# Kernel optimization log

Hardware: AMD Instinct MI355X
Metric: run time of the kernel (lower is better)

The kernel has to match this reference:

```python
import jax, jax.numpy as jnp
import numpy as np
import math

DIM = 512
HEADS = 8
HEAD_DIM = DIM // HEADS
WINDOW = 16
HIDDEN = 4 * DIM
SCALE = HEAD_DIM ** (-0.5)


def _best_hw(n):
    r = int(math.sqrt(n))
    best = (1, n)
    min_gap = n - 1
    for h in range(1, r + 1):
        if n % h == 0:
            w = n // h
            if abs(w - h) < min_gap:
                min_gap = abs(w - h)
                best = (h, w)
    return best


def _pad_to_window(x, w):
    # x: [B,C,H,W]
    B, C, H, W = x.shape
    ph = (-H) % w
    pw = (-W) % w
    if ph or pw:
        x = jnp.pad(x, ((0, 0), (0, 0), (0, ph), (0, pw)))
    return x, (ph, pw)


def _window_partition(x, w):
    # [B,C,Hp,Wp] -> [B*nW, w*w, C]
    B, C, Hp, Wp = x.shape
    x = x.reshape(B, C, Hp // w, w, Wp // w, w)
    x = jnp.transpose(x, (0, 2, 4, 3, 5, 1))  # [B,nWh,nWw,w,w,C]
    return x.reshape(-1, w * w, C), (Hp, Wp, Hp // w, Wp // w)


def _window_reverse(windows, w, meta):
    Hp, Wp, nWh, nWw = meta
    B = windows.shape[0] // (nWh * nWw)
    C = windows.shape[-1]
    x = windows.reshape(B, nWh, nWw, w, w, C)
    x = jnp.transpose(x, (0, 5, 1, 3, 2, 4))
    return x.reshape(B, C, Hp, Wp)


def _branch(src, oth, Wq, bq, Wk, bk, Wv, bv, Wo, bo, W1, b1, W2, b2):
    # src acts as query grid; oth is resized onto src's grid (cross attention)
    B, N, C = src.shape
    Hs, Ws = _best_hw(N)
    src_map = jnp.transpose(src, (0, 2, 1)).reshape(B, C, Hs, Ws)
    M = oth.shape[1]
    Ho, Wo_sp = _best_hw(M)
    oth_map = jnp.transpose(oth, (0, 2, 1)).reshape(B, C, Ho, Wo_sp)
    # bilinear resize, half-pixel centers (== torch align_corners=False, no antialias)
    oth_rs = jax.image.resize(oth_map, (B, C, Hs, Ws), method='bilinear', antialias=False)

    src_pad, (ph, pw) = _pad_to_window(src_map, WINDOW)
    oth_pad, _ = _pad_to_window(oth_rs, WINDOW)
    src_win, meta = _window_partition(src_pad, WINDOW)   # [Bn,T,C]
    oth_win, _ = _window_partition(oth_pad, WINDOW)

    q = src_win @ Wq + bq
    k = oth_win @ Wk + bk
    v = src_win @ Wv + bv
    Bn, T, _ = q.shape
    q = q.reshape(Bn, T, HEADS, HEAD_DIM)
    k = k.reshape(Bn, T, HEADS, HEAD_DIM)
    v = v.reshape(Bn, T, HEADS, HEAD_DIM)
    attn = jnp.einsum('bthd,bshd->bhts', q, k) * SCALE
    attn = jax.nn.softmax(attn, axis=-1)  # dropout is identity in eval
    out = jnp.einsum('bhts,bshd->bthd', attn, v).reshape(Bn, T, C)
    out = out @ Wo + bo

    out_map = _window_reverse(out, WINDOW, meta)
    Hp, Wp = out_map.shape[-2:]
    if ph or pw:
        out_map = out_map[:, :, :Hp - ph, :Wp - pw]
    tokens = jnp.transpose(out_map.reshape(B, C, -1), (0, 2, 1)) + src
    # MLP (GELU exact, dropout identity)
    h = jax.nn.gelu(tokens @ W1 + b1, approximate=False)
    tokens = (h @ W2 + b2) + tokens
    return tokens


def setup_inputs() -> dict:
    key = jax.random.key(0)
    ks = jax.random.split(key, 16)
    s = 0.02
    return {
        'x': jax.random.normal(ks[0], (8, 4096, DIM), jnp.float32),
        'y': jax.random.normal(ks[1], (8, 1024, DIM), jnp.float32),
        'Wq': jax.random.normal(ks[2], (DIM, DIM), jnp.float32) * s,
        'bq': jnp.zeros((DIM,), jnp.float32),
        'Wk': jax.random.normal(ks[3], (DIM, DIM), jnp.float32) * s,
        'bk': jnp.zeros((DIM,), jnp.float32),
        'Wv': jax.random.normal(ks[4], (DIM, DIM), jnp.float32) * s,
        'bv': jnp.zeros((DIM,), jnp.float32),
        'Wo': jax.random.normal(ks[5], (DIM, DIM), jnp.float32) * s,
        'bo': jnp.zeros((DIM,), jnp.float32),
        'W1': jax.random.normal(ks[6], (DIM, HIDDEN), jnp.float32) * s,
        'b1': jnp.zeros((HIDDEN,), jnp.float32),
        'W2': jax.random.normal(ks[7], (HIDDEN, DIM), jnp.float32) * s,
        'b2': jnp.zeros((DIM,), jnp.float32),
    }


def reference(x, y, Wq, bq, Wk, bk, Wv, bv, Wo, bo, W1, b1, W2, b2):
    out_x = _branch(x, y, Wq, bq, Wk, bk, Wv, bv, Wo, bo, W1, b1, W2, b2)
    out_y = _branch(y, x, Wq, bq, Wk, bk, Wv, bv, Wo, bo, W1, b1, W2, b2)
    return jnp.concatenate([out_x, out_y], axis=1)  # [B, N+M, C]
```

## Files before the change

### kernel.cpp

```cpp
#include <hip/hip_runtime.h>
#include <hip/hip_bf16.h>
#include <math.h>

typedef __attribute__((ext_vector_type(8))) __bf16 bf8_t;
typedef __attribute__((ext_vector_type(4))) float f4_t;
typedef __attribute__((ext_vector_type(4))) int   i4_t;

#define XTOK 32768
#define NTOK 40960
#define DIMC 512

__device__ __forceinline__ void gload_lds16(const __bf16* g, __bf16* l) {
  __builtin_amdgcn_global_load_lds((const __attribute__((address_space(1))) void*)g,
                                   (__attribute__((address_space(3))) void*)l, 16, 0, 0);
}
__device__ __forceinline__ float bflo(unsigned u) { union { unsigned x; float f; } c; c.x = u << 16; return c.f; }
__device__ __forceinline__ float bfhi(unsigned u) { union { unsigned x; float f; } c; c.x = u & 0xffff0000u; return c.f; }

__device__ __forceinline__ float gelu_fast(float v) {
  float u = v * 0.70710678118654752f;
  float a = fabsf(u);
  float t = __builtin_amdgcn_rcpf(1.0f + 0.3275911f * a);
  float e = __builtin_amdgcn_exp2f(-a * a * 1.4426950408889634f);
  float poly = t * (0.254829592f + t * (-0.284496736f + t * (1.421413741f +
               t * (-1.453152027f + t * 1.061405429f))));
  float erfa = 1.0f - poly * e;
  float erfu = (u < 0.0f) ? -erfa : erfa;
  return 0.5f * v * (1.0f + erfu);
}

__global__ void transpose_all(const float* __restrict__ Wq, const float* __restrict__ Wv,
                              const float* __restrict__ Wk, const float* __restrict__ Wo,
                              const float* __restrict__ W1, const float* __restrict__ W2,
                              __bf16* __restrict__ WqvT, __bf16* __restrict__ WkT,
                              __bf16* __restrict__ WoT, __bf16* __restrict__ W1T,
                              __bf16* __restrict__ W2T) {
  __shared__ float t[32][33];
  int b = blockIdx.x;
  const float* W; __bf16* WT; int K, N, tb;
  if (b < 256)       { W = Wq; WT = WqvT;                       K = 512;  N = 512;  tb = b; }
  else if (b < 512)  { W = Wv; WT = WqvT + (size_t)512 * 512;   K = 512;  N = 512;  tb = b - 256; }
  else if (b < 768)  { W = Wk; WT = WkT;                        K = 512;  N = 512;  tb = b - 512; }
  else if (b < 1024) { W = Wo; WT = WoT;                        K = 512;  N = 512;  tb = b - 768; }
  else if (b < 2048) { W = W1; WT = W1T;                        K = 512;  N = 2048; tb = b - 1024; }
  else               { W = W2; WT = W2T;                        K = 2048; N = 512;  tb = b - 2048; }
  int ntn = N >> 5;
  int bk = (tb / ntn) * 32, bn = (tb - (tb / ntn) * ntn) * 32;
  int tx = threadIdx.x & 31, ty = threadIdx.x >> 5;
#pragma unroll
  for (int i = 0; i < 4; ++i)
    t[ty + i * 8][tx] = W[(size_t)(bk + ty + i * 8) * N + bn + tx];
  __syncthreads();
#pragma unroll
  for (int i = 0; i < 4; ++i)
    WT[(size_t)(bn + ty + i * 8) * K + bk + tx] = (__bf16)t[tx][ty + i * 8];
}

__global__ void pack_tokens(const float* __restrict__ x, const float* __restrict__ y,
                            __bf16* __restrict__ Asrc, __bf16* __restrict__ Aoth,
                            int* __restrict__ srcoff, int* __restrict__ outoff) {
  int g = blockIdx.x;
  int t = threadIdx.x;
  int b, h, w; int soff, ooff; bool isx = (g < XTOK);
  if (isx) {
    b = g >> 12;
    int w5 = g & 4095;
    int widx = w5 >> 8, tt = w5 & 255;
    int wh = widx >> 2, ww = widx & 3;
    h = wh * 16 + (tt >> 4); w = ww * 16 + (tt & 15);
    int n = h * 64 + w;
    soff = (b * 4096 + n) * 512;
    ooff = (b * 5120 + n) * 512;
  } else {
    int gy = g - XTOK;
    b = gy >> 10;
    int w5 = gy & 1023;
    int widx = w5 >> 8, tt = w5 & 255;
    int wh = widx >> 1, ww = widx & 1;
    h = wh * 16 + (tt >> 4); w = ww * 16 + (tt & 15);
    int n = h * 32 + w;
    soff = (b * 1024 + n) * 512;
    ooff = (b * 5120 + 4096 + n) * 512;
  }
  if (t == 0) { srcoff[g] = soff; outoff[g] = ooff; }
  const float* sp = (isx ? x : y) + (size_t)soff + t * 2;
  float2 sv = *(const float2*)sp;
  size_t gb = (size_t)g * 512 + t * 2;
  Asrc[gb]     = (__bf16)sv.x;
  Asrc[gb + 1] = (__bf16)sv.y;

  float o0, o1;
  if (isx) {
    int h0, h1, w0i, w1i; float fh0, fh1, fw0, fw1;
    if (h & 1) { h0 = h >> 1; h1 = (h0 + 1 < 31) ? h0 + 1 : 31; fh0 = 0.75f; fh1 = 0.25f; }
    else       { h1 = h >> 1; h0 = (h1 - 1 > 0) ? h1 - 1 : 0;   fh0 = 0.25f; fh1 = 0.75f; }
    if (w & 1) { w0i = w >> 1; w1i = (w0i + 1 < 31) ? w0i + 1 : 31; fw0 = 0.75f; fw1 = 0.25f; }
    else       { w1i = w >> 1; w0i = (w1i - 1 > 0) ? w1i - 1 : 0;   fw0 = 0.25f; fw1 = 0.75f; }
    const float* yb = y + (size_t)b * 1024 * 512 + t * 2;
    float2 v00 = *(const float2*)(yb + (h0 * 32 + w0i) * 512);
    float2 v01 = *(const float2*)(yb + (h0 * 32 + w1i) * 512);
    float2 v10 = *(const float2*)(yb + (h1 * 32 + w0i) * 512);
    float2 v11 = *(const float2*)(yb + (h1 * 32 + w1i) * 512);
    o0 = fh0 * (fw0 * v00.x + fw1 * v01.x) + fh1 * (fw0 * v10.x + fw1 * v11.x);
    o1 = fh0 * (fw0 * v00.y + fw1 * v01.y) + fh1 * (fw0 * v10.y + fw1 * v11.y);
  } else {
    const float* xb = x + (size_t)b * 4096 * 512 + t * 2;
    float2 v00 = *(const float2*)(xb + ((2 * h) * 64 + 2 * w) * 512);
    float2 v01 = *(const float2*)(xb + ((2 * h) * 64 + 2 * w + 1) * 512);
    float2 v10 = *(const float2*)(xb + ((2 * h + 1) * 64 + 2 * w) * 512);
    float2 v11 = *(const float2*)(xb + ((2 * h + 1) * 64 + 2 * w + 1) * 512);
    o0 = 0.25f * (v00.x + v01.x + v10.x + v11.x);
    o1 = 0.25f * (v00.y + v01.y + v10.y + v11.y);
  }
  Aoth[gb]     = (__bf16)o0;
  Aoth[gb + 1] = (__bf16)o1;
}

template<int EPI>
__global__ __launch_bounds__(256, 2)
void gemm_bt(const __bf16* __restrict__ A, const __bf16* __restrict__ BT,
             const float* __restrict__ bias, const float* __restrict__ bias2,
             int K, int nbn, int row0,
             __bf16* __restrict__ outb, __bf16* __restrict__ outb2,
             const float* __restrict__ resx, const float* __restrict__ resy,
             const int* __restrict__ srcoff, const int* __restrict__ outoff,
             const __bf16* __restrict__ toksr, float* __restrict__ dout) {
  const int N = nbn * 128;
  __shared__ __align__(16) __bf16 smem[17408];
  int nwg = gridDim.x;
  int qq = nwg >> 3, rr = nwg & 7;
  int xcd = blockIdx.x & 7, base = blockIdx.x >> 3;
  int wg = (xcd < rr ? xcd * (qq + 1) : rr * (qq + 1) + (xcd - rr) * qq) + base;
  int bm = wg / nbn, bn = wg - bm * nbn;
  int m0 = bm * 128, n0 = bn * 128;

  int tid = threadIdx.x, lane = tid & 63, wid = tid >> 6;
  int wr = wid >> 1, wc = wid & 1;
  int ln15 = lane & 15, kq = lane >> 4;

  f4_t acc[4][4];
#pragma unroll
  for (int m = 0; m < 4; ++m)
#pragma unroll
    for (int n = 0; n < 4; ++n) acc[m][n] = f4_t{0.f, 0.f, 0.f, 0.f};

  int offA[4], offB[4];
#pragma unroll
  for (int m = 0; m < 4; ++m) {
    int row = wr * 64 + m * 16 + ln15;
    offA[m] = row * 32 + ((kq ^ (row & 3) ^ ((row >> 2) & 3)) << 3);
  }
#pragma unroll
  for (int n = 0; n < 4; ++n) {
    int row = wc * 64 + n * 16 + ln15;
    offB[n] = 4096 + row * 32 + ((kq ^ (row & 3) ^ ((row >> 2) & 3)) << 3);
  }
  int srow[2], scol[2], sdst[2];
#pragma unroll
  for (int j = 0; j < 2; ++j) {
    int ci = (wid * 2 + j) * 64 + lane;
    int row = ci >> 2;
    srow[j] = row;
    scol[j] = ((ci & 3) ^ (row & 3) ^ ((row >> 2) & 3)) * 8;
    sdst[j] = (wid * 2 + j) * 512;
  }

  auto stage = [&](int slotbase, int kt) {
    int k0 = kt << 5;
#pragma unroll
    for (int j = 0; j < 2; ++j) {
      gload_lds16(A  + (size_t)(m0 + srow[j]) * K + k0 + scol[j], &smem[slotbase + sdst[j]]);
      gload_lds16(BT + (size_t)(n0 + srow[j]) * K + k0 + scol[j], &smem[slotbase + 4096 + sdst[j]]);
    }
  };

#define GEMM_HALF(SLOTBASE)                                                       \
  do {                                                                            \
    bf8_t av[4], bv[4];                                                           \
    _Pragma("unroll")                                                             \
    for (int m = 0; m < 4; ++m) av[m] = *(const bf8_t*)&smem[(SLOTBASE) + offA[m]]; \
    _Pragma("unroll")                                                             \
    for (int n = 0; n < 4; ++n) bv[n] = *(const bf8_t*)&smem[(SLOTBASE) + offB[n]]; \
    __builtin_amdgcn_s_setprio(1);                                                \
    _Pragma("unroll")                                                             \
    for (int m = 0; m < 4; ++m) {                                                 \
      _Pragma("unroll")                                                           \
      for (int n = 0; n < 4; ++n)                                                 \
        acc[m][n] = __builtin_amdgcn_mfma_f32_16x16x32_bf16(av[m], bv[n], acc[m][n], 0, 0, 0); \
    }                                                                             \
    __builtin_amdgcn_s_setprio(0);                                                \
  } while (0)

  int nt = K >> 5;
  stage(0, 0);
  __syncthreads();
  for (int t = 0; t < nt; t += 2) {
    stage(8192, t + 1);
    GEMM_HALF(0);
    __syncthreads();
    if (t + 2 < nt) stage(0, t + 2);
    GEMM_HALF(8192);
    __syncthreads();
  }
#undef GEMM_HALF

  bool hi = (EPI == 4) && (n0 >= 512);
  const float* bptr = hi ? bias2 : bias;
  int nbase = hi ? n0 - 512 : n0;
  float bs[4];
#pragma unroll
  for (int n = 0; n < 4; ++n) bs[n] = bptr[nbase + wc * 64 + n * 16 + ln15];

#pragma unroll
  for (int m = 0; m < 4; ++m) {
    int lr2 = m0 + wr * 64 + m * 16 + kq * 4;
#pragma unroll
    for (int r = 0; r < 4; ++r) {
      int grow = row0 + lr2 + r;
      const float* rptr = nullptr; int so = 0;
      if (EPI == 1) { so = srcoff[grow]; rptr = (grow < XTOK) ? resx : resy; }
#pragma unroll
      for (int n = 0; n < 4; ++n) {
        int gcol = nbase + wc * 64 + n * 16 + ln15;
        float v = acc[m][n][r] + bs[n];
        if (EPI == 1) v += rptr[(size_t)so + gcol];
        if (EPI == 2) v = gelu_fast(v);
        if (EPI == 3) v += (float)toksr[(size_t)grow * DIMC + gcol];
        acc[m][n][r] = v;
      }
    }
  }

  if (EPI != 3) {
#pragma unroll
    for (int m = 0; m < 4; ++m)
#pragma unroll
      for (int r = 0; r < 4; ++r)
#pragma unroll
        for (int n = 0; n < 4; ++n)
          smem[(wr * 64 + m * 16 + kq * 4 + r) * 136 + wc * 64 + n * 16 + ln15] = (__bf16)acc[m][n][r];
    __syncthreads();
    __bf16* ob = (EPI == 4 && hi) ? outb2 : outb;
    int ldn = (EPI == 2) ? N : 512;
    int gc0 = (EPI == 2) ? n0 : nbase;
#pragma unroll
    for (int it = 0; it < 8; ++it) {
      int cid = it * 256 + tid;
      int row = cid >> 4, c = cid & 15;
      i4_t v = *(const i4_t*)&smem[row * 136 + c * 8];
      *(i4_t*)&ob[(size_t)(m0 + row) * ldn + gc0 + c * 8] = v;
    }
  } else {
    float* stf = (float*)smem;
#pragma unroll
    for (int h = 0; h < 2; ++h) {
      __syncthreads();
      if (wc == h) {
#pragma unroll
        for (int m = 0; m < 4; ++m)
#pragma unroll
          for (int r = 0; r < 4; ++r)
#pragma unroll
            for (int n = 0; n < 4; ++n)
              stf[(wr * 64 + m * 16 + kq * 4 + r) * 68 + n * 16 + ln15] = acc[m][n][r];
      }
      __syncthreads();
#pragma unroll
      for (int it = 0; it < 8; ++it) {
        int cid = it * 256 + tid;
        int row = cid >> 4, c = cid & 15;
        f4_t v = *(const f4_t*)&stf[row * 68 + c * 4];
        int oo = outoff[row0 + m0 + row];
        *(f4_t*)&dout[(size_t)oo + n0 + h * 64 + c * 4] = v;
      }
    }
  }
}

__global__ __launch_bounds__(512, 2)
void attn_kernel(const __bf16* __restrict__ Qb, const __bf16* __restrict__ Kb,
                 const __bf16* __restrict__ Vb, __bf16* __restrict__ AOb) {
  __shared__ __align__(16) __bf16 smem[32768];
  __bf16* Kl = smem;
  __bf16* Vt = smem + 16384;
  int tid = threadIdx.x, lane = tid & 63, wid = tid >> 6;
  int l15 = lane & 15, kq = lane >> 4;
  int win = blockIdx.x >> 3, head = blockIdx.x & 7;
  size_t wtok = (size_t)win * 256;
  int hc = head * 64;

#pragma unroll
  for (int it = 0; it < 4; ++it) {
    int i = (wid * 4 + it) * 64 + lane;
    int s = i >> 3, cp = i & 7, c = cp ^ (s & 7);
    gload_lds16(Kb + (wtok + s) * 512 + hc + c * 8, &Kl[(size_t)((wid * 4 + it) * 64) * 8]);
  }
#pragma unroll
  for (int it = 0; it < 4; ++it) {
    int j = tid + it * 512;
    int dc = j & 7, s = j >> 3;
    i4_t v = *(const i4_t*)(Vb + (wtok + s) * 512 + hc + dc * 8);
    const __bf16* ve = (const __bf16*)&v;
#pragma unroll
    for (int jj = 0; jj < 8; ++jj) {
      int d = dc * 8 + jj;
      int sc = (s >> 3) ^ (((d >> 3) ^ d) & 7);
      Vt[d * 256 + (sc << 3) + (s & 7)] = ve[jj];
    }
  }
  __syncthreads();

  const float CLOG2E = 0.18033688011112043f;
  f4_t oacc[2][4];
  float rinvq[2];
  int sl0 = ((kq & 1) << 5) + l15;
  int sl1 = sl0 + 16;
  bool hiT = (kq & 2) != 0;

#pragma unroll
  for (int qt = 0; qt < 2; ++qt) {
    int qbase = wid * 32 + qt * 16;
    bf8_t qf[2];
#pragma unroll
    for (int k2 = 0; k2 < 2; ++k2)
      qf[k2] = *(const bf8_t*)(Qb + (wtok + qbase + l15) * 512 + hc + k2 * 32 + kq * 8);

    uint2 ps[16];
    float mx = -3.0e38f;
    __builtin_amdgcn_s_setprio(1);
#pragma unroll
    for (int st = 0; st < 16; ++st) {
      f4_t z = {0.f, 0.f, 0.f, 0.f};
      int s = st * 16 + l15;
#pragma unroll
      for (int k2 = 0; k2 < 2; ++k2) {
        int c = (k2 * 4 + kq) ^ (s & 7);
        bf8_t kf = *(const bf8_t*)&Kl[(s * 8 + c) * 8];
        z = __builtin_amdgcn_mfma_f32_16x16x32_bf16(kf, qf[k2], z, 0, 0, 0);
      }
      z *= CLOG2E;
      mx = fmaxf(mx, fmaxf(fmaxf(z[0], z[1]), fmaxf(z[2], z[3])));
      union { __bf16 b[4]; uint2 u; } pk;
#pragma unroll
      for (int r = 0; r < 4; ++r) pk.b[r] = (__bf16)z[r];
      ps[st] = pk.u;
    }
    __builtin_amdgcn_s_setprio(0);
    mx = fmaxf(mx, __shfl_xor(mx, 16, 64));
    mx = fmaxf(mx, __shfl_xor(mx, 32, 64));

    float L = 0.f;
#pragma unroll
    for (int st = 0; st < 16; ++st) {
      uint2 u = ps[st];
      float p0 = __builtin_amdgcn_exp2f(bflo(u.x) - mx);
      float p1 = __builtin_amdgcn_exp2f(bfhi(u.x) - mx);
      float p2 = __builtin_amdgcn_exp2f(bflo(u.y) - mx);
      float p3 = __builtin_amdgcn_exp2f(bfhi(u.y) - mx);
      L += (p0 + p1) + (p2 + p3);
      union { __bf16 b[4]; uint2 u; } pk;
      pk.b[0] = (__bf16)p0; pk.b[1] = (__bf16)p1; pk.b[2] = (__bf16)p2; pk.b[3] = (__bf16)p3;
      ps[st] = pk.u;
    }
    L += __shfl_xor(L, 16, 64);
    L += __shfl_xor(L, 32, 64);
    rinvq[qt] = __builtin_amdgcn_rcpf(L);

#pragma unroll
    for (int dn = 0; dn < 4; ++dn) oacc[qt][dn] = f4_t{0.f, 0.f, 0.f, 0.f};
    __builtin_amdgcn_s_setprio(1);
#pragma unroll
    for (int c = 0; c < 8; ++c) {
      uint2 t0 = ps[2 * c], t1 = ps[2 * c + 1];
      int a00x = __shfl((int)t0.x, sl0, 64), a00y = __shfl((int)t0.y, sl0, 64);
      int a01x = __shfl((int)t0.x, sl1, 64), a01y = __shfl((int)t0.y, sl1, 64);
      int a10x = __shfl((int)t1.x, sl0, 64), a10y = __shfl((int)t1.y, sl0, 64);
      int a11x = __shfl((int)t1.x, sl1, 64), a11y = __shfl((int)t1.y, sl1, 64);
      union { int u[4]; bf8_t v; } fr;
      fr.u[0] = hiT ? a10x : a00x;
      fr.u[1] = hiT ? a10y : a00y;
      fr.u[2] = hiT ? a11x : a01x;
      fr.u[3] = hiT ? a11y : a01y;
#pragma unroll
      for (int dn = 0; dn < 4; ++dn) {
        int d = dn * 16 + l15;
        int sc = (4 * c + kq) ^ (((d >> 3) ^ d) & 7);
        bf8_t vf = *(const bf8_t*)&Vt[d * 256 + (sc << 3)];
        oacc[qt][dn] = __builtin_amdgcn_mfma_f32_16x16x32_bf16(fr.v, vf, oacc[qt][dn], 0, 0, 0);
      }
    }
    __builtin_amdgcn_s_setprio(0);
  }

  __syncthreads();
  __bf16* Ko = smem + wid * 2304;
#pragma unroll
  for (int qt = 0; qt < 2; ++qt)
#pragma unroll
    for (int dn = 0; dn < 4; ++dn)
#pragma unroll
      for (int r = 0; r < 4; ++r)
        Ko[(qt * 16 + kq * 4 + r) * 72 + dn * 16 + l15] = (__bf16)(oacc[qt][dn][r] * rinvq[qt]);
#pragma unroll
  for (int it = 0; it < 4; ++it) {
    int lr = it * 8 + (lane >> 3), cb = (lane & 7) * 8;
    i4_t v = *(const i4_t*)&Ko[lr * 72 + cb];
    *(i4_t*)&AOb[(wtok + wid * 32 + lr) * 512 + hc + cb] = v;
  }
}

extern "C" void kernel_launch(void* const* d_in, const int* in_sizes, int n_in,
                              void* d_out, int out_size, void* d_ws, size_t ws_size,
                              hipStream_t stream) {
  const float* x  = (const float*)d_in[0];
  const float* y  = (const float*)d_in[1];
  const float* Wq = (const float*)d_in[2];
  const float* bq = (const float*)d_in[3];
  const float* Wk = (const float*)d_in[4];
  const float* bk = (const float*)d_in[5];
  const float* Wv = (const float*)d_in[6];
  const float* bv = (const float*)d_in[7];
  const float* Wo = (const float*)d_in[8];
  const float* bo = (const float*)d_in[9];
  const float* W1 = (const float*)d_in[10];
  const float* b1 = (const float*)d_in[11];
  const float* W2 = (const float*)d_in[12];
  const float* b2 = (const float*)d_in[13];

  char* ws = (char*)d_ws;
  size_t off = 0;
  auto carve = [&](size_t bytes) -> void* {
    void* p = ws + off;
    off += (bytes + 255) & ~(size_t)255;
    return p;
  };
  __bf16* WqvT = (__bf16*)carve((size_t)1024 * 512 * 2);
  __bf16* WkT  = (__bf16*)carve((size_t)512 * 512 * 2);
  __bf16* WoT  = (__bf16*)carve((size_t)512 * 512 * 2);
  __bf16* W1T  = (__bf16*)carve((size_t)2048 * 512 * 2);
  __bf16* W2T  = (__bf16*)carve((size_t)512 * 2048 * 2);
  int* srcoff = (int*)carve((size_t)NTOK * 4);
  int* outoff = (int*)carve((size_t)NTOK * 4);
  __bf16* Asrc = (__bf16*)carve((size_t)NTOK * 512 * 2);
  __bf16* Aoth = (__bf16*)carve((size_t)NTOK * 512 * 2);
  __bf16* Qb   = (__bf16*)carve((size_t)NTOK * 512 * 2);
  __bf16* Kb   = (__bf16*)carve((size_t)NTOK * 512 * 2);
  __bf16* Vb   = (__bf16*)carve((size_t)NTOK * 512 * 2);
  int nc = 1;
  while (nc < 4 && off + (size_t)(NTOK / nc) * 2048 * 2 > ws_size) nc *= 2;
  int rows = NTOK / nc;
  __bf16* Hb = (__bf16*)carve((size_t)rows * 2048 * 2);
  __bf16* AOb   = Asrc;
  __bf16* toksb = Aoth;
  float*  dout  = (float*)d_out;

  transpose_all<<<3072, 256, 0, stream>>>(Wq, Wv, Wk, Wo, W1, W2, WqvT, WkT, WoT, W1T, W2T);

  pack_tokens<<<NTOK, 256, 0, stream>>>(x, y, Asrc, Aoth, srcoff, outoff);

  gemm_bt<4><<<NTOK / 128 * 8, 256, 0, stream>>>(Asrc, WqvT, bq, bv, 512, 8, 0, Qb, Vb, nullptr, nullptr, nullptr, nullptr, nullptr, nullptr);
  gemm_bt<0><<<NTOK / 128 * 4, 256, 0, stream>>>(Aoth, WkT, bk, nullptr, 512, 4, 0, Kb, nullptr, nullptr, nullptr, nullptr, nullptr, nullptr, nullptr);

  attn_kernel<<<160 * 8, 512, 0, stream>>>(Qb, Kb, Vb, AOb);

  gemm_bt<1><<<NTOK / 128 * 4, 256, 0, stream>>>(AOb, WoT, bo, nullptr, 512, 4, 0, toksb, nullptr, x, y, srcoff, nullptr, nullptr, nullptr);

  for (int c = 0; c < nc; ++c) {
    int r0 = c * rows;
    gemm_bt<2><<<rows / 128 * 16, 256, 0, stream>>>(toksb + (size_t)r0 * 512, W1T, b1, nullptr, 512, 16, r0, Hb, nullptr, nullptr, nullptr, nullptr, nullptr, nullptr, nullptr);
    gemm_bt<3><<<rows / 128 * 4, 256, 0, stream>>>(Hb, W2T, b2, nullptr, 2048, 4, r0, nullptr, nullptr, nullptr, nullptr, nullptr, outoff, toksb, dout);
  }
}
```

Before: 531.5 us.

## Triple-buffer GEMM k-loop and merge Q/V and K projections into one launch

```diff
diff --git a/kernel.cpp b/kernel.cpp
--- a/kernel.cpp
+++ b/kernel.cpp
@@ -124,14 +124,27 @@
              __bf16* __restrict__ outb, __bf16* __restrict__ outb2,
              const float* __restrict__ resx, const float* __restrict__ resy,
              const int* __restrict__ srcoff, const int* __restrict__ outoff,
-             const __bf16* __restrict__ toksr, float* __restrict__ dout) {
+             const __bf16* __restrict__ toksr, float* __restrict__ dout,
+             const __bf16* __restrict__ A2, const __bf16* __restrict__ BT2,
+             const float* __restrict__ bias3, __bf16* __restrict__ outb3) {
   const int N = nbn * 128;
-  __shared__ __align__(16) __bf16 smem[17408];
+  __shared__ __align__(16) __bf16 smem[24576];
   int nwg = gridDim.x;
   int qq = nwg >> 3, rr = nwg & 7;
   int xcd = blockIdx.x & 7, base = blockIdx.x >> 3;
   int wg = (xcd < rr ? xcd * (qq + 1) : rr * (qq + 1) + (xcd - rr) * qq) + base;
-  int bm = wg / nbn, bn = wg - bm * nbn;
+
+  bool isK = false;
+  int bm, bn;
+  const __bf16* Ap = A;
+  const __bf16* Bp = BT;
+  if (EPI == 5) {
+    isK = (wg >= row0);
+    if (isK) { int w2 = wg - row0; bm = w2 >> 2; bn = w2 & 3; Ap = A2; Bp = BT2; }
+    else     { bm = wg >> 3; bn = wg & 7; }
+  } else {
+    bm = wg / nbn; bn = wg - bm * nbn;
+  }
   int m0 = bm * 128, n0 = bn * 128;
 
   int tid = threadIdx.x, lane = tid & 63, wid = tid >> 6;
@@ -169,8 +182,8 @@
     int k0 = kt << 5;
 #pragma unroll
     for (int j = 0; j < 2; ++j) {
-      gload_lds16(A  + (size_t)(m0 + srow[j]) * K + k0 + scol[j], &smem[slotbase + sdst[j]]);
-      gload_lds16(BT + (size_t)(n0 + srow[j]) * K + k0 + scol[j], &smem[slotbase + 4096 + sdst[j]]);
+      gload_lds16(Ap + (size_t)(m0 + srow[j]) * K + k0 + scol[j], &smem[slotbase + sdst[j]]);
+      gload_lds16(Bp + (size_t)(n0 + srow[j]) * K + k0 + scol[j], &smem[slotbase + 4096 + sdst[j]]);
     }
   };
 
@@ -192,20 +205,28 @@
   } while (0)
 
   int nt = K >> 5;
-  stage(0, 0);
+  int rA = 0, rB = 8192, rC = 16384;
+  stage(rA, 0);
+  stage(rB, 1);
+  asm volatile("s_waitcnt vmcnt(4)" ::: "memory");
+  __builtin_amdgcn_s_barrier();
+  __builtin_amdgcn_sched_barrier(0);
+  for (int t = 0; t < nt; ++t) {
+    if (t + 2 < nt) stage(rC, t + 2);
+    GEMM_HALF(rA);
+    if (t + 1 < nt) {
+      if (t + 2 < nt) asm volatile("s_waitcnt vmcnt(4)" ::: "memory");
+      else            asm volatile("s_waitcnt vmcnt(0)" ::: "memory");
+      __builtin_amdgcn_s_barrier();
+      __builtin_amdgcn_sched_barrier(0);
+    }
+    int tmp = rA; rA = rB; rB = rC; rC = tmp;
+  }
+#undef GEMM_HALF
   __syncthreads();
-  for (int t = 0; t < nt; t += 2) {
-    stage(8192, t + 1);
-    GEMM_HALF(0);
-    __syncthreads();
-    if (t + 2 < nt) stage(0, t + 2);
-    GEMM_HALF(8192);
-    __syncthreads();
-  }
-#undef GEMM_HALF
-
-  bool hi = (EPI == 4) && (n0 >= 512);
-  const float* bptr = hi ? bias2 : bias;
+
+  bool hi = (EPI == 4 || EPI == 5) && !isK && (n0 >= 512);
+  const float* bptr = (EPI == 5 && isK) ? bias3 : (hi ? bias2 : bias);
   int nbase = hi ? n0 - 512 : n0;
   float bs[4];
 #pragma unroll
@@ -240,7 +261,7 @@
         for (int n = 0; n < 4; ++n)
           smem[(wr * 64 + m * 16 + kq * 4 + r) * 136 + wc * 64 + n * 16 + ln15] = (__bf16)acc[m][n][r];
     __syncthreads();
-    __bf16* ob = (EPI == 4 && hi) ? outb2 : outb;
+    __bf16* ob = (EPI == 5 && isK) ? outb3 : ((EPI == 4 || EPI == 5) && hi ? outb2 : outb);
     int ldn = (EPI == 2) ? N : 512;
     int gc0 = (EPI == 2) ? n0 : nbase;
 #pragma unroll
@@ -458,16 +479,21 @@
 
   pack_tokens<<<NTOK, 256, 0, stream>>>(x, y, Asrc, Aoth, srcoff, outoff);
 
-  gemm_bt<4><<<NTOK / 128 * 8, 256, 0, stream>>>(Asrc, WqvT, bq, bv, 512, 8, 0, Qb, Vb, nullptr, nullptr, nullptr, nullptr, nullptr, nullptr);
-  gemm_bt<0><<<NTOK / 128 * 4, 256, 0, stream>>>(Aoth, WkT, bk, nullptr, 512, 4, 0, Kb, nullptr, nullptr, nullptr, nullptr, nullptr, nullptr, nullptr);
+  gemm_bt<5><<<NTOK / 128 * 12, 256, 0, stream>>>(Asrc, WqvT, bq, bv, 512, 8, NTOK / 128 * 8,
+      Qb, Vb, nullptr, nullptr, nullptr, nullptr, nullptr, nullptr, Aoth, WkT, bk, Kb);
 
   attn_kernel<<<160 * 8, 512, 0, stream>>>(Qb, Kb, Vb, AOb);
 
-  gemm_bt<1><<<NTOK / 128 * 4, 256, 0, stream>>>(AOb, WoT, bo, nullptr, 512, 4, 0, toksb, nullptr, x, y, srcoff, nullptr, nullptr, nullptr);
+  gemm_bt<1><<<NTOK / 128 * 4, 256, 0, stream>>>(AOb, WoT, bo, nullptr, 512, 4, 0, toksb, nullptr,
+      x, y, srcoff, nullptr, nullptr, nullptr, nullptr, nullptr, nullptr, nullptr);
 
   for (int c = 0; c < nc; ++c) {
     int r0 = c * rows;
-    gemm_bt<2><<<rows / 128 * 16, 256, 0, stream>>>(toksb + (size_t)r0 * 512, W1T, b1, nullptr, 512, 16, r0, Hb, nullptr, nullptr, nullptr, nullptr, nullptr, nullptr, nullptr);
-    gemm_bt<3><<<rows / 128 * 4, 256, 0, stream>>>(Hb, W2T, b2, nullptr, 2048, 4, r0, nullptr, nullptr, nullptr, nullptr, nullptr, outoff, toksb, dout);
-  }
-}
+    gemm_bt<2><<<rows / 128 * 16, 256, 0, stream>>>(toksb + (size_t)r0 * 512, W1T, b1, nullptr,
+        512, 16, r0, Hb, nullptr, nullptr, nullptr, nullptr, nullptr, nullptr, nullptr,
+        nullptr, nullptr, nullptr, nullptr);
+    gemm_bt<3><<<rows / 128 * 4, 256, 0, stream>>>(Hb, W2T, b2, nullptr, 2048, 4, r0,
+        nullptr, nullptr, nullptr, nullptr, nullptr, outoff, toksb, dout,
+        nullptr, nullptr, nullptr, nullptr);
+  }
+}
```

New measurement: 543.3 us. 2.2% more time.
